# Kernel tuning notes

Measured on AMD Instinct MI355X. Metric: run time of the kernel, lower is better.

The kernel has to match this reference:

```python
import jax, jax.numpy as jnp
import numpy as np

B, T, C = 2, 2048, 2048
H, KVH, D = 16, 4, 128
EPS = 1.1920929e-07  # torch.finfo(float32).eps, default for F.rms_norm


def setup_inputs() -> dict:
    key = jax.random.key(0)
    ks = jax.random.split(key, 5)
    x = jax.random.normal(ks[0], (B, T, C), jnp.float32)
    # standard RoPE angle tables, shaped to broadcast over [B, T, heads, D/2]
    half = D // 2
    inv_freq = 1.0 / (10000.0 ** (np.arange(half, dtype=np.float64) / half))
    ang = np.arange(T, dtype=np.float64)[:, None] * inv_freq[None, :]
    cos = jnp.asarray(np.cos(ang), jnp.float32)[None, :, None, :]
    sin = jnp.asarray(np.sin(ang), jnp.float32)[None, :, None, :]
    s = C ** -0.5
    Wq = jax.random.normal(ks[1], (H * D, C), jnp.float32) * s
    Wk = jax.random.normal(ks[2], (KVH * D, C), jnp.float32) * s
    Wv = jax.random.normal(ks[3], (KVH * D, C), jnp.float32) * s
    Wo = jax.random.normal(ks[4], (C, C), jnp.float32) * s
    return {"x": x, "cos": cos, "sin": sin, "Wq": Wq, "Wk": Wk, "Wv": Wv, "Wo": Wo}


def _rope(x, cos, sin):
    d = x.shape[-1] // 2
    x1, x2 = x[..., :d], x[..., d:]
    return jnp.concatenate([x1 * cos + x2 * sin, -x1 * sin + x2 * cos], axis=-1)


def _rmsnorm(x):
    return x * jax.lax.rsqrt(jnp.mean(x * x, axis=-1, keepdims=True) + EPS)


def reference(x, cos, sin, Wq, Wk, Wv, Wo):
    Bx, Tx, Cx = x.shape
    q = (x @ Wq.T).reshape(Bx, Tx, H, D)
    k = (x @ Wk.T).reshape(Bx, Tx, KVH, D)
    v = (x @ Wv.T).reshape(Bx, Tx, KVH, D)
    q = _rmsnorm(_rope(q, cos, sin))
    k = _rmsnorm(_rope(k, cos, sin))
    # [B, heads, T, D]
    q = q.transpose(0, 2, 1, 3)
    k = k.transpose(0, 2, 1, 3)
    v = v.transpose(0, 2, 1, 3)
    groups = H // KVH  # GQA: replicate kv heads
    k = jnp.repeat(k, groups, axis=1)
    v = jnp.repeat(v, groups, axis=1)
    scale = 1.0 / jnp.sqrt(jnp.asarray(D, x.dtype))
    scores = jnp.einsum('bhqd,bhkd->bhqk', q, k) * scale
    causal = jnp.tril(jnp.ones((Tx, Tx), dtype=bool))
    scores = jnp.where(causal, scores, jnp.finfo(scores.dtype).min)
    att = jax.nn.softmax(scores, axis=-1)
    y = jnp.einsum('bhqk,bhkd->bhqd', att, v)
    y = y.transpose(0, 2, 1, 3).reshape(Bx, Tx, H * D)
    return y @ Wo.T
```

## Files before the change

### kernel.cpp

```cpp
#include <hip/hip_runtime.h>
#include <hip/hip_bf16.h>

typedef unsigned short u16t;
typedef unsigned int   u32t;
typedef float  f32x4 __attribute__((ext_vector_type(4)));
typedef short  s16x8 __attribute__((ext_vector_type(8)));
typedef unsigned int u32x4 __attribute__((ext_vector_type(4)));
typedef float  f4 __attribute__((ext_vector_type(4)));

#define BB 2
#define TT 2048
#define CC 2048
#define HH 16
#define KVHN 4
#define DD 128
#define EPSV 1.1920929e-07f
#define SCALE 0.08838834764831845f
#define MFIX 12.0f

__device__ __forceinline__ float b2f(u16t u){ union{u32t i; float f;} x; x.i=((u32t)u)<<16; return x.f; }
__device__ __forceinline__ u16t f2b(float f){ union{float f; u32t i;} x; x.f=f; u32t r = x.i + 0x7fffu + ((x.i>>16)&1u); return (u16t)(r>>16); }
__device__ __forceinline__ u32t pk2(float a, float b){
    __hip_bfloat162 h = __float22bfloat162_rn(make_float2(a,b));
    u32t r; __builtin_memcpy(&r,&h,4); return r;
}
__device__ __forceinline__ s16x8 ldf(const u16t* p){ s16x8 r; __builtin_memcpy(&r,p,16); return r; }
__device__ __forceinline__ void st16(u16t* p, u32x4 v){ __builtin_memcpy(p,&v,16); }
__device__ __forceinline__ u32x4 ldg16(const u16t* p){ u32x4 r; __builtin_memcpy(&r,p,16); return r; }

typedef const __attribute__((address_space(1))) unsigned int ga_u32;
typedef __attribute__((address_space(3))) unsigned int ls_u32;
__device__ __forceinline__ void gl16(const u16t* g, u16t* l) {
    __builtin_amdgcn_global_load_lds((ga_u32*)(unsigned long long)(g),
                                     (ls_u32*)(unsigned int)(unsigned long long)(l),
                                     16, 0, 0);
}

#define BARRIER() __builtin_amdgcn_s_barrier()
#define SCHEDB()  __builtin_amdgcn_sched_barrier(0)
#define WAITLG0() asm volatile("s_waitcnt lgkmcnt(0)" ::: "memory")
#define WAITVM8() asm volatile("s_waitcnt vmcnt(8)" ::: "memory")
#define WAITVM4() asm volatile("s_waitcnt vmcnt(4)" ::: "memory")
#define WAITVM0() asm volatile("s_waitcnt vmcnt(0)" ::: "memory")

__global__ __launch_bounds__(256) void cvt_kernel(
    const float* __restrict__ x,  const float* __restrict__ wq,
    const float* __restrict__ wk, const float* __restrict__ wv,
    const float* __restrict__ wo,
    u16t* __restrict__ xb, u16t* __restrict__ wqb, u16t* __restrict__ wkb,
    u16t* __restrict__ wvb, u16t* __restrict__ wob)
{
    size_t g = (size_t)blockIdx.x * 256 + threadIdx.x;
    const float* src; u16t* dst; size_t off;
    if      (g < 1048576) { src = x;  dst = xb;  off = g; }
    else if (g < 1572864) { src = wq; dst = wqb; off = g - 1048576; }
    else if (g < 1703936) { src = wk; dst = wkb; off = g - 1572864; }
    else if (g < 1835008) { src = wv; dst = wvb; off = g - 1703936; }
    else                  { src = wo; dst = wob; off = g - 1835008; }
    f4 a = *(const f4*)(src + off*8);
    f4 b = *(const f4*)(src + off*8 + 4);
    u32x4 o = { pk2(a[0],a[1]), pk2(a[2],a[3]), pk2(b[0],b[1]), pk2(b[2],b[3]) };
    st16(dst + off*8, o);
}

__device__ __forceinline__ void gemm256(
    const u16t* __restrict__ aPanel, const u16t* __restrict__ bPanel,
    u16t* lds, f32x4 (&acc)[4][8], const int tid)
{
    u16t* Abuf[2] = { lds,         lds + 32768 };
    u16t* Bbuf[2] = { lds + 16384, lds + 49152 };
    const int w = tid>>6, quad = (tid>>4)&3, l15 = tid&15;
    const int wr = (w>>1)*64, wc = (w&1)*128;
    const int gcol = (((tid&7) ^ ((tid>>3)&7)) << 3);
    const u16t* aB = aPanel + (size_t)(tid>>3)*CC + gcol;
    const u16t* bB = bPanel + (size_t)(tid>>3)*CC + gcol;

    #pragma unroll
    for (int i=0;i<4;++i)
        #pragma unroll
        for (int j=0;j<8;++j)
            #pragma unroll
            for (int r=0;r<4;++r) acc[i][j][r] = 0.f;

    #pragma unroll
    for (int i=0;i<4;++i){
        gl16(aB + (size_t)i*64*CC,      Abuf[0] + (i*512+tid)*8);
        gl16(bB + (size_t)i*64*CC,      Bbuf[0] + (i*512+tid)*8);
    }
    #pragma unroll
    for (int i=0;i<4;++i){
        gl16(aB + (size_t)i*64*CC + 64, Abuf[1] + (i*512+tid)*8);
        gl16(bB + (size_t)i*64*CC + 64, Bbuf[1] + (i*512+tid)*8);
    }

    s16x8 af[4], bf[4];
    #pragma unroll 2
    for (int kt=0; kt<32; ++kt){
        u16t* Ab = Abuf[kt&1];
        u16t* Bb = Bbuf[kt&1];
        if (kt == 31) { WAITVM0(); } else { WAITVM8(); }
        SCHEDB();
        BARRIER();
        #pragma unroll
        for (int ph=0; ph<4; ++ph){
            const int kh = ph>>1, nh = ph&1;
            if (nh == 0){
                #pragma unroll
                for (int mi=0;mi<4;++mi){
                    const int row = wr + mi*16 + l15;
                    af[mi] = ldf(Ab + row*64 + ((((kh<<2)|quad) ^ (row&7))<<3));
                }
            }
            #pragma unroll
            for (int ni=0;ni<4;++ni){
                const int row = wc + nh*64 + ni*16 + l15;
                bf[ni] = ldf(Bb + row*64 + ((((kh<<2)|quad) ^ (row&7))<<3));
            }
            BARRIER();
            WAITLG0();
            SCHEDB();
            __builtin_amdgcn_s_setprio(1);
            #pragma unroll
            for (int mi=0;mi<4;++mi)
                #pragma unroll
                for (int ni=0;ni<4;++ni)
                    acc[mi][(nh<<2)|ni] = __builtin_amdgcn_mfma_f32_16x16x32_bf16(
                        af[mi], bf[ni], acc[mi][(nh<<2)|ni], 0,0,0);
            __builtin_amdgcn_s_setprio(0);
            SCHEDB();
            BARRIER();
        }
        if (kt < 30){
            const int k0 = (kt+2)*64;
            #pragma unroll
            for (int i=0;i<4;++i){
                gl16(aB + (size_t)i*64*CC + k0, Ab + (i*512+tid)*8);
                gl16(bB + (size_t)i*64*CC + k0, Bb + (i*512+tid)*8);
            }
        }
    }
}

__global__ __launch_bounds__(512,2) void qkv_kernel(
    const u16t* __restrict__ xb, const u16t* __restrict__ wqb,
    const u16t* __restrict__ wkb, const u16t* __restrict__ wvb,
    const float* __restrict__ cosp, const float* __restrict__ sinp,
    u16t* __restrict__ qws, u16t* __restrict__ kws, u16t* __restrict__ vtw)
{
    __shared__ u16t lds[65536];
    const int tid = threadIdx.x;
    const int bx = blockIdx.x, by = blockIdx.y;
    const int m0 = bx*256;

    int type, headbase; const u16t* W;
    if (by < 8)       { type=0; W = wqb + (size_t)by*256*CC;      headbase = by*2; }
    else if (by < 10) { type=1; W = wkb + (size_t)(by-8)*256*CC;  headbase = (by-8)*2; }
    else              { type=2; W = wvb + (size_t)(by-10)*256*CC; headbase = (by-10)*2; }

    f32x4 acc[4][8];
    gemm256(xb + (size_t)m0*CC, W, lds, acc, tid);

    const int w = tid>>6, quad = (tid>>4)&3, l15 = tid&15;
    const int wr = (w>>1)*64, wn = w&1;
    const int head = headbase + wn;
    const int bb = bx>>3;
    const int ttb = (m0 + wr) & 2047;

    if (type == 2){
        u16t* vb = vtw + (size_t)(bb*KVHN+head)*DD*TT;
        #pragma unroll
        for (int mi=0;mi<4;++mi){
            const int tt = ttb + mi*16 + quad*4;
            #pragma unroll
            for (int ni=0;ni<8;++ni){
                const int d = ni*16 + l15;
                u16t o[4];
                #pragma unroll
                for (int r=0;r<4;++r) o[r] = f2b(acc[mi][ni][r]);
                __builtin_memcpy(vb + (size_t)d*TT + tt, o, 8);
            }
        }
    } else {
        u16t* dst = (type==0) ? (qws + (size_t)(bb*HH+head)*TT*DD)
                              : (kws + (size_t)(bb*KVHN+head)*TT*DD);
        #pragma unroll
        for (int mi=0;mi<4;++mi){
            const int tt0 = ttb + mi*16 + quad*4;
            float ss[4] = {0.f,0.f,0.f,0.f};
            #pragma unroll
            for (int ni=0;ni<8;++ni)
                #pragma unroll
                for (int r=0;r<4;++r) ss[r] += acc[mi][ni][r]*acc[mi][ni][r];
            float rms[4];
            #pragma unroll
            for (int r=0;r<4;++r){
                float s = ss[r];
                s += __shfl_xor(s, 1, 16);
                s += __shfl_xor(s, 2, 16);
                s += __shfl_xor(s, 4, 16);
                s += __shfl_xor(s, 8, 16);
                rms[r] = rsqrtf(s*(1.f/128.f) + EPSV);
            }
            #pragma unroll
            for (int ni=0;ni<4;++ni){
                const int j = ni*16 + l15;
                #pragma unroll
                for (int r=0;r<4;++r){
                    const int tt = tt0 + r;
                    const float c = cosp[tt*64 + j];
                    const float s = sinp[tt*64 + j];
                    const float z1 = acc[mi][ni][r], z2 = acc[mi][ni+4][r];
                    dst[(size_t)tt*DD + j]      = f2b((z1*c + z2*s)*rms[r]);
                    dst[(size_t)tt*DD + j + 64] = f2b((z2*c - z1*s)*rms[r]);
                }
            }
        }
    }
}

__global__ __launch_bounds__(512,2) void attn_kernel(
    const u16t* __restrict__ qws, const u16t* __restrict__ kws,
    const u16t* __restrict__ vtw, u16t* __restrict__ yws)
{
    __shared__ u16t lds[49152];
    u16t* Ps = lds + 32768;

    const int tid = threadIdx.x;
    const int w = tid>>6, lane = tid&63, quad = lane>>4, l15 = lane&15;
    const int bx = blockIdx.x, h = blockIdx.y, b = blockIdx.z, kvh = h>>2;

    const int qti    = (w < 4) ? (15 - bx) : bx;
    const int qwbase = qti*128 + (w&3)*32;
    const int nkt    = (16 - bx)*2;

    const u16t* kb = kws + (size_t)(b*KVHN+kvh)*TT*DD;
    const u16t* vb = vtw + (size_t)(b*KVHN+kvh)*DD*TT;

    const int krow = tid>>4;
    const int kcg  = (tid&15) ^ ((tid>>4)&7);
    const int vrow = tid>>3;
    const int vcg  = (tid&7)  ^ ((tid>>3)&7);

    const u16t* qp = qws + ((size_t)(b*HH+h)*TT + qwbase + l15)*DD + quad*8;
    s16x8 qf[2][4];
    #pragma unroll
    for (int mi=0;mi<2;++mi)
        #pragma unroll
        for (int kq=0;kq<4;++kq)
            qf[mi][kq] = ldf(qp + (size_t)mi*16*DD + kq*32);

    {
        u16t* Kd = lds;        u16t* Vd = lds + 16384;
        gl16(kb + (size_t)(krow)*DD + kcg*8,        Kd + tid*8);
        gl16(kb + (size_t)(krow+32)*DD + kcg*8,     Kd + (512+tid)*8);
        gl16(vb + (size_t)(vrow)*TT + vcg*8,        Vd + tid*8);
        gl16(vb + (size_t)(vrow+64)*TT + vcg*8,     Vd + (512+tid)*8);
        SCHEDB();
        Kd = lds + 8192;       Vd = lds + 24576;
        gl16(kb + (size_t)(krow+64)*DD + kcg*8,      Kd + tid*8);
        gl16(kb + (size_t)(krow+96)*DD + kcg*8,      Kd + (512+tid)*8);
        gl16(vb + (size_t)(vrow)*TT + 64 + vcg*8,    Vd + tid*8);
        gl16(vb + (size_t)(vrow+64)*TT + 64 + vcg*8, Vd + (512+tid)*8);
    }

    f32x4 o_[2][8];
    float l_[2][4];
    #pragma unroll
    for (int mi=0;mi<2;++mi){
        #pragma unroll
        for (int r=0;r<4;++r) l_[mi][r] = 0.f;
        #pragma unroll
        for (int n8=0;n8<8;++n8)
            #pragma unroll
            for (int r=0;r<4;++r) o_[mi][n8][r] = 0.f;
    }

    const int swz = (l15&7)<<3;

    for (int kt=0; kt<nkt; ++kt){
        const int k0 = kt*64;
        if (kt+1 == nkt) { WAITVM0(); } else { WAITVM4(); }
        SCHEDB();
        BARRIER();
        if (k0 <= qwbase + 31) {
            const u16t* Ks = (kt&1) ? (lds + 8192)  : lds;
            const u16t* Vt = (kt&1) ? (lds + 24576) : (lds + 16384);

            f32x4 s[2][4];
            #pragma unroll
            for (int mi=0;mi<2;++mi)
                #pragma unroll
                for (int ni=0;ni<4;++ni)
                    #pragma unroll
                    for (int r=0;r<4;++r) s[mi][ni][r] = 0.f;
            #pragma unroll
            for (int kq=0;kq<4;++kq){
                s16x8 kf[4];
                #pragma unroll
                for (int ni=0;ni<4;++ni)
                    kf[ni] = ldf(Ks + (ni*16+l15)*128 + (((kq*4+quad)<<3) ^ swz));
                __builtin_amdgcn_s_setprio(1);
                #pragma unroll
                for (int mi=0;mi<2;++mi)
                    #pragma unroll
                    for (int ni=0;ni<4;++ni)
                        s[mi][ni] = __builtin_amdgcn_mfma_f32_16x16x32_bf16(qf[mi][kq], kf[ni], s[mi][ni], 0,0,0);
                __builtin_amdgcn_s_setprio(0);
            }

            const bool need_mask = (k0 + 63) > qwbase;
            #pragma unroll
            for (int mi=0;mi<2;++mi){
                const int qrow = qwbase + mi*16 + quad*4;
                #pragma unroll
                for (int ni=0;ni<4;++ni){
                    const int kcol = k0 + ni*16 + l15;
                    #pragma unroll
                    for (int r=0;r<4;++r){
                        float p = __expf(__builtin_fmaf(s[mi][ni][r], SCALE, -MFIX));
                        if (need_mask && kcol > qrow + r) p = 0.f;
                        l_[mi][r] += p;
                        const int rw = w*32 + mi*16 + quad*4 + r;
                        Ps[rw*64 + ((ni*16+l15) ^ (((quad*4+r)&7)<<3))] = f2b(p);
                    }
                }
            }

            #pragma unroll
            for (int ks=0;ks<2;++ks){
                s16x8 pf[2];
                #pragma unroll
                for (int mi=0;mi<2;++mi)
                    pf[mi] = ldf(Ps + (w*32+mi*16+l15)*64 + (((ks*4+quad)<<3) ^ swz));
                __builtin_amdgcn_s_setprio(1);
                #pragma unroll
                for (int n8=0;n8<8;++n8){
                    s16x8 vf = ldf(Vt + (n8*16+l15)*64 + (((ks*4+quad)<<3) ^ swz));
                    #pragma unroll
                    for (int mi=0;mi<2;++mi)
                        o_[mi][n8] = __builtin_amdgcn_mfma_f32_16x16x32_bf16(pf[mi], vf, o_[mi][n8], 0,0,0);
                }
                __builtin_amdgcn_s_setprio(0);
            }
        }
        BARRIER();
        if (kt+2 < nkt){
            const int kn = (kt+2)*64;
            u16t* Kd = (kt&1) ? (lds + 8192)  : lds;
            u16t* Vd = (kt&1) ? (lds + 24576) : (lds + 16384);
            gl16(kb + (size_t)(kn+krow)*DD + kcg*8,      Kd + tid*8);
            gl16(kb + (size_t)(kn+krow+32)*DD + kcg*8,   Kd + (512+tid)*8);
            gl16(vb + (size_t)(vrow)*TT + kn + vcg*8,    Vd + tid*8);
            gl16(vb + (size_t)(vrow+64)*TT + kn + vcg*8, Vd + (512+tid)*8);
        }
    }

    #pragma unroll
    for (int mi=0;mi<2;++mi){
        const int qrow = qwbase + mi*16 + quad*4;
        float inv[4];
        #pragma unroll
        for (int r=0;r<4;++r){
            float lt = l_[mi][r];
            lt += __shfl_xor(lt,1,16);
            lt += __shfl_xor(lt,2,16);
            lt += __shfl_xor(lt,4,16);
            lt += __shfl_xor(lt,8,16);
            inv[r] = 1.f/lt;
        }
        #pragma unroll
        for (int n8=0;n8<8;++n8)
            #pragma unroll
            for (int r=0;r<4;++r)
                yws[((size_t)(b*TT + qrow + r))*2048 + h*DD + n8*16 + l15] = f2b(o_[mi][n8][r]*inv[r]);
    }
}

__global__ __launch_bounds__(512,2) void oproj_kernel(
    const u16t* __restrict__ y, const u16t* __restrict__ wob, float* __restrict__ out)
{
    __shared__ u16t lds[65536];
    const int tid = threadIdx.x;
    const int m0 = blockIdx.x*256, n0 = blockIdx.y*256;

    f32x4 acc[4][8];
    gemm256(y + (size_t)m0*CC, wob + (size_t)n0*CC, lds, acc, tid);

    const int w = tid>>6, quad = (tid>>4)&3, l15 = tid&15;
    const int wr = (w>>1)*64, wc = (w&1)*128;
    #pragma unroll
    for (int mi=0;mi<4;++mi){
        const int m = m0 + wr + mi*16 + quad*4;
        #pragma unroll
        for (int ni=0;ni<8;++ni){
            const int n = n0 + wc + ni*16 + l15;
            #pragma unroll
            for (int r=0;r<4;++r)
                out[(size_t)(m+r)*CC + n] = acc[mi][ni][r];
        }
    }
}

extern "C" void kernel_launch(void* const* d_in, const int* in_sizes, int n_in,
                              void* d_out, int out_size, void* d_ws, size_t ws_size,
                              hipStream_t stream) {
    const float* x    = (const float*)d_in[0];
    const float* cosp = (const float*)d_in[1];
    const float* sinp = (const float*)d_in[2];
    const float* Wq   = (const float*)d_in[3];
    const float* Wk   = (const float*)d_in[4];
    const float* Wv   = (const float*)d_in[5];
    const float* Wo   = (const float*)d_in[6];

    u16t* ws  = (u16t*)d_ws;
    u16t* xb  = ws;
    u16t* wqb = xb  + 8388608;
    u16t* wkb = wqb + 4194304;
    u16t* wvb = wkb + 1048576;
    u16t* wob = wvb + 1048576;
    u16t* qws = wob + 4194304;
    u16t* kws = qws + 8388608;
    u16t* vtw = kws + 2097152;
    u16t* yws = xb;
    float* out = (float*)d_out;

    cvt_kernel<<<dim3(9216), 256, 0, stream>>>(x, Wq, Wk, Wv, Wo, xb, wqb, wkb, wvb, wob);
    qkv_kernel<<<dim3(16, 12), 512, 0, stream>>>(xb, wqb, wkb, wvb, cosp, sinp, qws, kws, vtw);
    attn_kernel<<<dim3(8, 16, 2), 512, 0, stream>>>(qws, kws, vtw, yws);
    oproj_kernel<<<dim3(16, 8), 512, 0, stream>>>(yws, wob, out);
}
```

Measured before the change: 341.3 us.

## Pipeline LDS fragment loads with MFMA and shrink oproj tile to 256x128

After: 355.5 us. +4.2%, slower.

```diff
diff --git a/kernel.cpp b/kernel.cpp
--- a/kernel.cpp
+++ b/kernel.cpp
@@ -39,7 +39,12 @@
 #define BARRIER() __builtin_amdgcn_s_barrier()
 #define SCHEDB()  __builtin_amdgcn_sched_barrier(0)
 #define WAITLG0() asm volatile("s_waitcnt lgkmcnt(0)" ::: "memory")
+#define WAITLG2() asm volatile("s_waitcnt lgkmcnt(2)" ::: "memory")
+#define WAITLG4() asm volatile("s_waitcnt lgkmcnt(4)" ::: "memory")
+#define WAITLG6() asm volatile("s_waitcnt lgkmcnt(6)" ::: "memory")
+#define WAITLG8() asm volatile("s_waitcnt lgkmcnt(8)" ::: "memory")
 #define WAITVM8() asm volatile("s_waitcnt vmcnt(8)" ::: "memory")
+#define WAITVM6() asm volatile("s_waitcnt vmcnt(6)" ::: "memory")
 #define WAITVM4() asm volatile("s_waitcnt vmcnt(4)" ::: "memory")
 #define WAITVM0() asm volatile("s_waitcnt vmcnt(0)" ::: "memory")
 
@@ -63,14 +68,16 @@
     st16(dst + off*8, o);
 }
 
+template<int NF>
 __device__ __forceinline__ void gemm256(
     const u16t* __restrict__ aPanel, const u16t* __restrict__ bPanel,
-    u16t* lds, f32x4 (&acc)[4][8], const int tid)
+    u16t* lds, f32x4 (&acc)[4][NF], const int tid)
 {
-    u16t* Abuf[2] = { lds,         lds + 32768 };
-    u16t* Bbuf[2] = { lds + 16384, lds + 49152 };
+    constexpr int BQ = NF/2;
+    u16t* Abuf[2] = { lds,         lds + 16384 };
+    u16t* Bbuf[2] = { lds + 32768, lds + 32768 + NF*2048 };
     const int w = tid>>6, quad = (tid>>4)&3, l15 = tid&15;
-    const int wr = (w>>1)*64, wc = (w&1)*128;
+    const int wr = (w>>1)*64, wc = (w&1)*(NF*16);
     const int gcol = (((tid&7) ^ ((tid>>3)&7)) << 3);
     const u16t* aB = aPanel + (size_t)(tid>>3)*CC + gcol;
     const u16t* bB = bPanel + (size_t)(tid>>3)*CC + gcol;
@@ -78,65 +85,112 @@
     #pragma unroll
     for (int i=0;i<4;++i)
         #pragma unroll
-        for (int j=0;j<8;++j)
+        for (int j=0;j<NF;++j)
             #pragma unroll
             for (int r=0;r<4;++r) acc[i][j][r] = 0.f;
 
     #pragma unroll
-    for (int i=0;i<4;++i){
-        gl16(aB + (size_t)i*64*CC,      Abuf[0] + (i*512+tid)*8);
-        gl16(bB + (size_t)i*64*CC,      Bbuf[0] + (i*512+tid)*8);
-    }
-    #pragma unroll
-    for (int i=0;i<4;++i){
-        gl16(aB + (size_t)i*64*CC + 64, Abuf[1] + (i*512+tid)*8);
-        gl16(bB + (size_t)i*64*CC + 64, Bbuf[1] + (i*512+tid)*8);
-    }
-
-    s16x8 af[4], bf[4];
+    for (int i=0;i<4;++i)  gl16(aB + (size_t)(i*64)*CC,      Abuf[0] + (i*512+tid)*8);
+    #pragma unroll
+    for (int i=0;i<BQ;++i) gl16(bB + (size_t)(i*64)*CC,      Bbuf[0] + (i*512+tid)*8);
+    SCHEDB();
+    #pragma unroll
+    for (int i=0;i<4;++i)  gl16(aB + (size_t)(i*64)*CC + 64, Abuf[1] + (i*512+tid)*8);
+    #pragma unroll
+    for (int i=0;i<BQ;++i) gl16(bB + (size_t)(i*64)*CC + 64, Bbuf[1] + (i*512+tid)*8);
+
+    s16x8 afr[2][4];
+    s16x8 bfr[3][BQ];
+
     #pragma unroll 2
     for (int kt=0; kt<32; ++kt){
-        u16t* Ab = Abuf[kt&1];
-        u16t* Bb = Bbuf[kt&1];
-        if (kt == 31) { WAITVM0(); } else { WAITVM8(); }
+        const u16t* Ac = Abuf[kt&1];
+        const u16t* Bc = Bbuf[kt&1];
+        if (kt == 31) { WAITVM0(); }
+        else { if constexpr (NF==8) { WAITVM8(); } else { WAITVM6(); } }
         SCHEDB();
         BARRIER();
-        #pragma unroll
-        for (int ph=0; ph<4; ++ph){
-            const int kh = ph>>1, nh = ph&1;
-            if (nh == 0){
-                #pragma unroll
-                for (int mi=0;mi<4;++mi){
-                    const int row = wr + mi*16 + l15;
-                    af[mi] = ldf(Ab + row*64 + ((((kh<<2)|quad) ^ (row&7))<<3));
-                }
-            }
-            #pragma unroll
-            for (int ni=0;ni<4;++ni){
-                const int row = wc + nh*64 + ni*16 + l15;
-                bf[ni] = ldf(Bb + row*64 + ((((kh<<2)|quad) ^ (row&7))<<3));
-            }
-            BARRIER();
-            WAITLG0();
-            SCHEDB();
-            __builtin_amdgcn_s_setprio(1);
-            #pragma unroll
-            for (int mi=0;mi<4;++mi)
-                #pragma unroll
-                for (int ni=0;ni<4;++ni)
-                    acc[mi][(nh<<2)|ni] = __builtin_amdgcn_mfma_f32_16x16x32_bf16(
-                        af[mi], bf[ni], acc[mi][(nh<<2)|ni], 0,0,0);
-            __builtin_amdgcn_s_setprio(0);
-            SCHEDB();
-            BARRIER();
-        }
+
+        #pragma unroll
+        for (int mi=0;mi<4;++mi){
+            const int row = wr + mi*16 + l15;
+            afr[0][mi] = ldf(Ac + row*64 + ((quad ^ (row&7))<<3));
+        }
+        #pragma unroll
+        for (int ni=0;ni<BQ;++ni){
+            const int row = wc + ni*16 + l15;
+            bfr[0][ni] = ldf(Bc + row*64 + ((quad ^ (row&7))<<3));
+        }
+        SCHEDB();
+        #pragma unroll
+        for (int ni=0;ni<BQ;++ni){
+            const int row = wc + BQ*16 + ni*16 + l15;
+            bfr[1][ni] = ldf(Bc + row*64 + ((quad ^ (row&7))<<3));
+        }
+        if constexpr (NF==8) { WAITLG4(); } else { WAITLG2(); }
+        SCHEDB();
+        __builtin_amdgcn_s_setprio(1);
+        #pragma unroll
+        for (int mi=0;mi<4;++mi)
+            #pragma unroll
+            for (int ni=0;ni<BQ;++ni)
+                acc[mi][ni] = __builtin_amdgcn_mfma_f32_16x16x32_bf16(
+                    afr[0][mi], bfr[0][ni], acc[mi][ni], 0,0,0);
+        __builtin_amdgcn_s_setprio(0);
+        #pragma unroll
+        for (int mi=0;mi<4;++mi){
+            const int row = wr + mi*16 + l15;
+            afr[1][mi] = ldf(Ac + row*64 + (((4|quad) ^ (row&7))<<3));
+        }
+        #pragma unroll
+        for (int ni=0;ni<BQ;++ni){
+            const int row = wc + ni*16 + l15;
+            bfr[2][ni] = ldf(Bc + row*64 + (((4|quad) ^ (row&7))<<3));
+        }
+        if constexpr (NF==8) { WAITLG8(); } else { WAITLG6(); }
+        SCHEDB();
+        __builtin_amdgcn_s_setprio(1);
+        #pragma unroll
+        for (int mi=0;mi<4;++mi)
+            #pragma unroll
+            for (int ni=0;ni<BQ;++ni)
+                acc[mi][BQ+ni] = __builtin_amdgcn_mfma_f32_16x16x32_bf16(
+                    afr[0][mi], bfr[1][ni], acc[mi][BQ+ni], 0,0,0);
+        __builtin_amdgcn_s_setprio(0);
+        #pragma unroll
+        for (int ni=0;ni<BQ;++ni){
+            const int row = wc + BQ*16 + ni*16 + l15;
+            bfr[0][ni] = ldf(Bc + row*64 + (((4|quad) ^ (row&7))<<3));
+        }
+        if constexpr (NF==8) { WAITLG4(); } else { WAITLG2(); }
+        SCHEDB();
+        __builtin_amdgcn_s_setprio(1);
+        #pragma unroll
+        for (int mi=0;mi<4;++mi)
+            #pragma unroll
+            for (int ni=0;ni<BQ;++ni)
+                acc[mi][ni] = __builtin_amdgcn_mfma_f32_16x16x32_bf16(
+                    afr[1][mi], bfr[2][ni], acc[mi][ni], 0,0,0);
+        __builtin_amdgcn_s_setprio(0);
+        WAITLG0();
+        SCHEDB();
+        __builtin_amdgcn_s_setprio(1);
+        #pragma unroll
+        for (int mi=0;mi<4;++mi)
+            #pragma unroll
+            for (int ni=0;ni<BQ;++ni)
+                acc[mi][BQ+ni] = __builtin_amdgcn_mfma_f32_16x16x32_bf16(
+                    afr[1][mi], bfr[0][ni], acc[mi][BQ+ni], 0,0,0);
+        __builtin_amdgcn_s_setprio(0);
+
+        BARRIER();
         if (kt < 30){
             const int k0 = (kt+2)*64;
-            #pragma unroll
-            for (int i=0;i<4;++i){
-                gl16(aB + (size_t)i*64*CC + k0, Ab + (i*512+tid)*8);
-                gl16(bB + (size_t)i*64*CC + k0, Bb + (i*512+tid)*8);
-            }
+            u16t* Ad = Abuf[kt&1]; u16t* Bd = Bbuf[kt&1];
+            #pragma unroll
+            for (int i=0;i<4;++i)  gl16(aB + (size_t)(i*64)*CC + k0, Ad + (i*512+tid)*8);
+            #pragma unroll
+            for (int i=0;i<BQ;++i) gl16(bB + (size_t)(i*64)*CC + k0, Bd + (i*512+tid)*8);
         }
     }
 }
@@ -147,7 +201,7 @@
     const float* __restrict__ cosp, const float* __restrict__ sinp,
     u16t* __restrict__ qws, u16t* __restrict__ kws, u16t* __restrict__ vtw)
 {
-    __shared__ u16t lds[65536];
+    __shared__ __align__(16) u16t lds[65536];
     const int tid = threadIdx.x;
     const int bx = blockIdx.x, by = blockIdx.y;
     const int m0 = bx*256;
@@ -158,7 +212,7 @@
     else              { type=2; W = wvb + (size_t)(by-10)*256*CC; headbase = (by-10)*2; }
 
     f32x4 acc[4][8];
-    gemm256(xb + (size_t)m0*CC, W, lds, acc, tid);
+    gemm256<8>(xb + (size_t)m0*CC, W, lds, acc, tid);
 
     const int w = tid>>6, quad = (tid>>4)&3, l15 = tid&15;
     const int wr = (w>>1)*64, wn = w&1;
@@ -222,7 +276,7 @@
     const u16t* __restrict__ qws, const u16t* __restrict__ kws,
     const u16t* __restrict__ vtw, u16t* __restrict__ yws)
 {
-    __shared__ u16t lds[49152];
+    __shared__ __align__(16) u16t lds[49152];
     u16t* Ps = lds + 32768;
 
     const int tid = threadIdx.x;
@@ -379,20 +433,20 @@
 __global__ __launch_bounds__(512,2) void oproj_kernel(
     const u16t* __restrict__ y, const u16t* __restrict__ wob, float* __restrict__ out)
 {
-    __shared__ u16t lds[65536];
+    __shared__ __align__(16) u16t lds[49152];
     const int tid = threadIdx.x;
-    const int m0 = blockIdx.x*256, n0 = blockIdx.y*256;
-
-    f32x4 acc[4][8];
-    gemm256(y + (size_t)m0*CC, wob + (size_t)n0*CC, lds, acc, tid);
+    const int m0 = blockIdx.x*256, n0 = blockIdx.y*128;
+
+    f32x4 acc[4][4];
+    gemm256<4>(y + (size_t)m0*CC, wob + (size_t)n0*CC, lds, acc, tid);
 
     const int w = tid>>6, quad = (tid>>4)&3, l15 = tid&15;
-    const int wr = (w>>1)*64, wc = (w&1)*128;
+    const int wr = (w>>1)*64, wc = (w&1)*64;
     #pragma unroll
     for (int mi=0;mi<4;++mi){
         const int m = m0 + wr + mi*16 + quad*4;
         #pragma unroll
-        for (int ni=0;ni<8;++ni){
+        for (int ni=0;ni<4;++ni){
             const int n = n0 + wc + ni*16 + l15;
             #pragma unroll
             for (int r=0;r<4;++r)
@@ -427,5 +481,5 @@
     cvt_kernel<<<dim3(9216), 256, 0, stream>>>(x, Wq, Wk, Wv, Wo, xb, wqb, wkb, wvb, wob);
     qkv_kernel<<<dim3(16, 12), 512, 0, stream>>>(xb, wqb, wkb, wvb, cosp, sinp, qws, kws, vtw);
     attn_kernel<<<dim3(8, 16, 2), 512, 0, stream>>>(qws, kws, vtw, yws);
-    oproj_kernel<<<dim3(16, 8), 512, 0, stream>>>(yws, wob, out);
-}
+    oproj_kernel<<<dim3(16, 16), 512, 0, stream>>>(yws, wob, out);
+}
```
